# Optimization experiments

Hardware: AMD Instinct MI355X
Metric: run time of the kernel (lower is better)

Reference implementation:

```python
import jax, jax.numpy as jnp
import numpy as np

KERNEL_SIZE = 4
N_QUBITS = KERNEL_SIZE ** 2  # 16 qubits -> 2**16 statevector
THRESHOLD = 0.0


def _apply_rx(state, theta, q, n):
    """Apply RX(theta_b) on qubit q for every batch element.
    state: (B, 2**n) complex64, theta: (B,) float32. Qiskit little-endian:
    bit q of the flat index has stride 2**q."""
    B = state.shape[0]
    outer, inner = 2 ** (n - q - 1), 2 ** q
    s = state.reshape(B, outer, 2, inner)
    c = jnp.cos(theta * 0.5).astype(state.dtype)[:, None, None]
    ms = (-1j * jnp.sin(theta * 0.5).astype(state.dtype))[:, None, None]
    s0, s1 = s[:, :, 0, :], s[:, :, 1, :]
    new = jnp.stack([c * s0 + ms * s1, ms * s0 + c * s1], axis=2)
    return new.reshape(B, -1)


def _apply_cx(state, q, n):
    """CX with control=q, target=q+1 (adjacent bits)."""
    B = state.shape[0]
    outer, inner = 2 ** (n - q - 2), 2 ** q
    # axes: (B, high bits, target bit q+1, control bit q, low bits)
    s = state.reshape(B, outer, 2, 2, inner)
    ctrl0 = s[:, :, :, 0, :]
    ctrl1 = s[:, :, ::-1, 1, :]  # flip target amplitude when control=1
    new = jnp.stack([ctrl0, ctrl1], axis=3)
    return new.reshape(B, -1)


def quantum_expectation(flat):
    """Exact (infinite-shot) expectation of the measured circuit:
    H^n |0..0>, RX(theta_i) per qubit, CX chain, exp = P(q0=1) - P(q0=0)
    (the torch code scores bitstr[-1]=='1' as +1). theta_i = pi if
    flat_i > threshold else 0 (non-differentiable threshold binarization)."""
    B, n = flat.shape
    thetas = jax.lax.stop_gradient(
        jnp.where(flat > THRESHOLD, jnp.pi, 0.0).astype(jnp.float32))
    dim = 2 ** n
    # after H on every qubit the state is uniform: amplitude 2**(-n/2)
    state = jnp.full((B, dim), 2.0 ** (-n / 2), dtype=jnp.complex64)
    for q in range(n):
        state = _apply_rx(state, thetas[:, q], q, n)
    for q in range(n - 1):
        state = _apply_cx(state, q, n)
    probs = state.real ** 2 + state.imag ** 2
    p1 = probs.reshape(B, dim // 2, 2)[:, :, 1].sum(axis=1)  # qubit 0 = stride-1 bit
    return 2.0 * p1 - 1.0


def setup_inputs() -> dict:
    key = jax.random.key(0)
    k1, k2, k3 = jax.random.split(key, 3)
    data = jax.random.normal(k1, (256, 1, 64, 64), dtype=jnp.float32)
    conv_w = jax.random.normal(k2, (1, 1, KERNEL_SIZE, KERNEL_SIZE), dtype=jnp.float32) * 0.5
    conv_b = jax.random.normal(k3, (1,), dtype=jnp.float32) * 0.1
    return {"data": data, "conv_w": conv_w, "conv_b": conv_b}


def reference(data, conv_w, conv_b):
    # classical branch: conv2d (valid) + sigmoid(logits - threshold), global mean
    logits = jax.lax.conv_general_dilated(
        data, conv_w, window_strides=(1, 1), padding='VALID',
        dimension_numbers=('NCHW', 'OIHW', 'NCHW')) + conv_b[None, :, None, None]
    classical_mean = jax.nn.sigmoid(logits - THRESHOLD).mean()
    # quantum branch: first n_qubits flattened pixels per sample
    B = data.shape[0]
    flat = data.reshape(B, -1)[:, :N_QUBITS]
    qexp = quantum_expectation(flat)
    return 0.5 * classical_mean + 0.5 * qexp  # shape (B,)
```

## Files before the change

kernel.cpp:

```cpp
#include <hip/hip_runtime.h>


constexpr int IMG   = 64;
constexpr int OUTW  = 61;
constexpr int NPIX  = OUTW * OUTW;
constexpr int BATCH = 256;
constexpr int GPR   = 16;
constexpr int NGRP  = OUTW * GPR;
constexpr float INV_TOTAL = 1.0f / (float)(BATCH * NPIX);

__device__ __forceinline__ float sigf(float s) {
    return __builtin_amdgcn_rcpf(1.0f + __expf(-s));
}

__global__ __launch_bounds__(256) void conv_sig_partial(
    const float* __restrict__ data, const float* __restrict__ w,
    const float* __restrict__ bias, float* __restrict__ ws)
{
    __shared__ __align__(16) float img[IMG * IMG + 4];
    __shared__ float wsm[16];
    __shared__ float wave_part[4];

    const int tid = threadIdx.x;

    const float* src = data + (size_t)blockIdx.x * (IMG * IMG);
    #pragma unroll
    for (int i = 0; i < 4; ++i)
        reinterpret_cast<float4*>(img)[tid + 256 * i] =
            reinterpret_cast<const float4*>(src)[tid + 256 * i];
    if (tid < 16) wsm[tid] = w[tid];
    if (tid >= 16 && tid < 20) img[IMG * IMG + tid - 16] = 0.0f;
    __syncthreads();

    float wr[16];
    #pragma unroll
    for (int k = 0; k < 16; ++k) wr[k] = wsm[k];
    const float b0 = bias[0];

    const float4* imgv = reinterpret_cast<const float4*>(img);
    float acc = 0.0f;

    for (int gidx = tid; gidx < NGRP; gidx += 256) {
        const int i = gidx >> 4;
        const int g = gidx & 15;
        float s0 = b0, s1 = b0, s2 = b0, s3 = b0;
        #pragma unroll
        for (int ki = 0; ki < 4; ++ki) {
            const int rb = (i + ki) * (IMG / 4) + g;
            const float4 a = imgv[rb];
            const float4 c = imgv[rb + 1];
            const float w0 = wr[ki * 4 + 0], w1 = wr[ki * 4 + 1];
            const float w2 = wr[ki * 4 + 2], w3 = wr[ki * 4 + 3];
            s0 = fmaf(a.x, w0, fmaf(a.y, w1, fmaf(a.z, w2, fmaf(a.w, w3, s0))));
            s1 = fmaf(a.y, w0, fmaf(a.z, w1, fmaf(a.w, w2, fmaf(c.x, w3, s1))));
            s2 = fmaf(a.z, w0, fmaf(a.w, w1, fmaf(c.x, w2, fmaf(c.y, w3, s2))));
            s3 = fmaf(a.w, w0, fmaf(c.x, w1, fmaf(c.y, w2, fmaf(c.z, w3, s3))));
        }
        if (g == 15) {
            acc += sigf(s0);
        } else {
            acc += sigf(s0) + sigf(s1) + sigf(s2) + sigf(s3);
        }
    }

    #pragma unroll
    for (int off = 32; off > 0; off >>= 1)
        acc += __shfl_down(acc, off, 64);
    if ((tid & 63) == 0) wave_part[tid >> 6] = acc;
    __syncthreads();

    if (tid == 0)
        ws[blockIdx.x] = wave_part[0] + wave_part[1] + wave_part[2] + wave_part[3];
}

__global__ __launch_bounds__(256) void reduce_broadcast(
    const float* __restrict__ ws, float* __restrict__ out)
{
    __shared__ float wave_part[4];
    __shared__ float result;

    const int tid = threadIdx.x;
    float acc = ws[tid];
    #pragma unroll
    for (int off = 32; off > 0; off >>= 1)
        acc += __shfl_down(acc, off, 64);
    if ((tid & 63) == 0) wave_part[tid >> 6] = acc;
    __syncthreads();
    if (tid == 0) {
        float total = wave_part[0] + wave_part[1] + wave_part[2] + wave_part[3];
        result = 0.5f * (total * INV_TOTAL);
    }
    __syncthreads();
    out[tid] = result;
}

extern "C" void kernel_launch(void* const* d_in, const int* in_sizes, int n_in,
                              void* d_out, int out_size, void* d_ws, size_t ws_size,
                              hipStream_t stream)
{
    const float* data = (const float*)d_in[0];
    const float* w    = (const float*)d_in[1];
    const float* bias = (const float*)d_in[2];
    float* out = (float*)d_out;
    float* ws  = (float*)d_ws;

    conv_sig_partial<<<BATCH, 256, 0, stream>>>(data, w, bias, ws);
    reduce_broadcast<<<1, 256, 0, stream>>>(ws, out);
}
```

Measured before the change: 60.87 us.

## Fuse conv partials and final reduction with a cooperative grid sync

Merges the two kernel launches into a single cooperative kernel. Each block writes its partial sum, a grid-wide sync follows, and block 0 then reduces the partials and broadcasts the result. This removes the second launch and the gap between kernels, but adds the cost of a grid barrier and a cooperative launch. If the cooperative launch fails it falls back to the original two-kernel path.

```diff
diff --git a/kernel.cpp b/kernel.cpp
--- a/kernel.cpp
+++ b/kernel.cpp
@@ -1,4 +1,7 @@
 #include <hip/hip_runtime.h>
+#include <hip/hip_cooperative_groups.h>
+
+namespace cg = cooperative_groups;
 
 
 constexpr int IMG   = 64;
@@ -13,9 +16,9 @@
     return __builtin_amdgcn_rcpf(1.0f + __expf(-s));
 }
 
-__global__ __launch_bounds__(256) void conv_sig_partial(
+__device__ __forceinline__ float conv_partial(
     const float* __restrict__ data, const float* __restrict__ w,
-    const float* __restrict__ bias, float* __restrict__ ws)
+    const float* __restrict__ bias)
 {
     __shared__ __align__(16) float img[IMG * IMG + 4];
     __shared__ float wsm[16];
@@ -69,8 +72,43 @@
     if ((tid & 63) == 0) wave_part[tid >> 6] = acc;
     __syncthreads();
 
+    return wave_part[0] + wave_part[1] + wave_part[2] + wave_part[3];
+}
+
+__global__ __launch_bounds__(256) void conv_sig_coop(
+    const float* __restrict__ data, const float* __restrict__ w,
+    const float* __restrict__ bias, float* __restrict__ ws,
+    float* __restrict__ out)
+{
+    const int tid = threadIdx.x;
+    const float p = conv_partial(data, w, bias);
+    if (tid == 0) ws[blockIdx.x] = p;
+
+    cg::this_grid().sync();
+
+    if (blockIdx.x != 0) return;
+
+    __shared__ float wave_part2[4];
+    __shared__ float bcast;
+    float v = ws[tid];
+    #pragma unroll
+    for (int off = 32; off > 0; off >>= 1)
+        v += __shfl_down(v, off, 64);
+    if ((tid & 63) == 0) wave_part2[tid >> 6] = v;
+    __syncthreads();
     if (tid == 0)
-        ws[blockIdx.x] = wave_part[0] + wave_part[1] + wave_part[2] + wave_part[3];
+        bcast = 0.5f * ((wave_part2[0] + wave_part2[1] +
+                         wave_part2[2] + wave_part2[3]) * INV_TOTAL);
+    __syncthreads();
+    out[tid] = bcast;
+}
+
+__global__ __launch_bounds__(256) void conv_sig_partial(
+    const float* __restrict__ data, const float* __restrict__ w,
+    const float* __restrict__ bias, float* __restrict__ ws)
+{
+    const float p = conv_partial(data, w, bias);
+    if (threadIdx.x == 0) ws[blockIdx.x] = p;
 }
 
 __global__ __launch_bounds__(256) void reduce_broadcast(
@@ -104,6 +142,13 @@
     float* out = (float*)d_out;
     float* ws  = (float*)d_ws;
 
-    conv_sig_partial<<<BATCH, 256, 0, stream>>>(data, w, bias, ws);
-    reduce_broadcast<<<1, 256, 0, stream>>>(ws, out);
+    void* args[] = { (void*)&data, (void*)&w, (void*)&bias,
+                     (void*)&ws, (void*)&out };
+    hipError_t err = hipLaunchCooperativeKernel(
+        (void*)conv_sig_coop, dim3(BATCH), dim3(256), args, 0, stream);
+
+    if (err != hipSuccess) {
+        conv_sig_partial<<<BATCH, 256, 0, stream>>>(data, w, bias, ws);
+        reduce_broadcast<<<1, 256, 0, stream>>>(ws, out);
+    }
 }
```

Result: slower. 92.81 us (+52.5%).
